# Optimization experiments

Hardware: AMD Instinct MI355X
Metric: run time of the kernel (lower is better)

The kernel has to match this reference:

```python
import jax, jax.numpy as jnp
import numpy as np

EPS = 1e-5

def _mesh_conv_point(f, nbr, w, b):
    # f: [B, C, V] features; nbr: [B, V, K] neighbor vertex indices
    # gather neighbor features per batch: [B, C, V, K]
    g = jax.vmap(lambda fb, nb: fb[:, nb])(f, nbr)
    # prepend self feature -> [B, C, V, K+1]
    x = jnp.concatenate([f[:, :, :, None], g], axis=3)
    # Conv2d with kernel (1, K+1) == contraction over (C, K+1)
    return jnp.einsum('bcvk,ock->bov', x, w) + b[None, :, None]

def _instance_norm(y):
    # InstanceNorm2d (affine=False): normalize over spatial dims (V, 1)
    m = jnp.mean(y, axis=2, keepdims=True)
    v = jnp.var(y, axis=2, keepdims=True)
    return (y - m) * jax.lax.rsqrt(v + EPS)

def setup_inputs() -> dict:
    key = jax.random.key(0)
    k1, k2, k3, k4 = jax.random.split(key, 4)
    B, Cin, Cout, V, K = 4, 64, 128, 50000, 6
    fe = jax.random.normal(k1, (B, Cin, V), dtype=jnp.float32)
    nbrs = jax.random.randint(k2, (B, V, K), 0, V, dtype=jnp.int32)
    w1 = jax.random.normal(k3, (Cout, Cin, K + 1), dtype=jnp.float32) * (1.0 / np.sqrt(Cin * (K + 1)))
    b1 = jnp.zeros((Cout,), dtype=jnp.float32)
    w2 = jax.random.normal(k4, (Cout, Cout, K + 1), dtype=jnp.float32) * (1.0 / np.sqrt(Cout * (K + 1)))
    b2 = jnp.zeros((Cout,), dtype=jnp.float32)
    return {"fe": fe, "nbrs": nbrs, "w1": w1, "b1": b1, "w2": w2, "b2": b2}

def reference(fe, nbrs, w1, b1, w2, b2):
    # conv1 -> instance norm -> relu
    x1 = jax.nn.relu(_instance_norm(_mesh_conv_point(fe, nbrs, w1, b1)))
    # residual block: conv2 -> instance norm -> + x1 -> relu
    x2 = jax.nn.relu(_instance_norm(_mesh_conv_point(x1, nbrs, w2, b2)) + x1)
    # pool=0, so output == before_pool; return the single [B, Cout, V] tensor
    return x2
```

## Files before the change

### kernel.cpp

```cpp
#include <hip/hip_runtime.h>
#include <cstdint>
#include <cstddef>
#include <utility>

typedef unsigned short u16;
typedef u16 u16x8 __attribute__((ext_vector_type(8)));
typedef u16 u16x4 __attribute__((ext_vector_type(4)));
typedef _Float16 f16x8 __attribute__((ext_vector_type(8)));
typedef float f32x4 __attribute__((ext_vector_type(4)));

constexpr int B    = 4;
constexpr int CIN  = 64;
constexpr int COUT = 128;
constexpr int V    = 50000;
constexpr int KP1  = 7;
constexpr float EPS = 1e-5f;

constexpr int BN   = 128;
constexpr int NT   = (V + BN - 1) / BN;
constexpr int NTP  = 392;
constexpr int NT64 = (V + 63) / 64;

__device__ __forceinline__ u16 f2h(float f) {
    _Float16 h = (_Float16)f;
    return __builtin_bit_cast(u16, h);
}
__device__ __forceinline__ float h2f(u16 s) {
    return (float)__builtin_bit_cast(_Float16, s);
}

__device__ __forceinline__ void relusub8(u16x8& a, const u16x8& m) {
    f16x8 af = __builtin_bit_cast(f16x8, a);
    f16x8 mf = __builtin_bit_cast(f16x8, m);
    f16x8 r = af - mf;
#pragma unroll
    for (int j = 0; j < 8; ++j)
        r[j] = (r[j] > (_Float16)0.f) ? r[j] : (_Float16)0.f;
    a = __builtin_bit_cast(u16x8, r);
}

template<int... Is, typename F>
__device__ __forceinline__ void static_for_impl(F&& f, std::integer_sequence<int, Is...>) {
    (f(std::integral_constant<int, Is>{}), ...);
}
template<int N, typename F>
__device__ __forceinline__ void static_for(F&& f) {
    static_for_impl(f, std::make_integer_sequence<int, N>{});
}

template<int C>
__global__ __launch_bounds__(256) void prep_wf(const float* __restrict__ w,
                                               u16* __restrict__ wF) {
    constexpr int RCH = KP1 * C / 32;
    const int g = blockIdx.x * 256 + threadIdx.x;
    if (g >= RCH * 8 * 64) return;
    const int l  = g & 63;
    const int m  = (g >> 6) & 7;
    const int ch = g >> 9;
    const int k  = ch / (C / 32);
    const int c0 = (ch % (C / 32)) * 32;
    const int o  = m * 16 + (l & 15);
    u16x8 out;
#pragma unroll
    for (int j = 0; j < 8; ++j) {
        const int c = c0 + (l >> 4) * 8 + j;
        out[j] = f2h(w[((size_t)o * C + c) * KP1 + k]);
    }
    *(u16x8*)&wF[(size_t)g * 8] = out;
}

__global__ __launch_bounds__(256) void prep_wf_inv(const float* __restrict__ w,
                                                   const float2* __restrict__ S1,
                                                   u16* __restrict__ wF) {
    constexpr int C = COUT;
    constexpr int RCH = KP1 * C / 32;
    const int g  = blockIdx.x * 256 + threadIdx.x;
    const int bb = blockIdx.y;
    if (g >= RCH * 8 * 64) return;
    const int l  = g & 63;
    const int m  = (g >> 6) & 7;
    const int ch = g >> 9;
    const int k  = ch / (C / 32);
    const int c0 = (ch % (C / 32)) * 32;
    const int o  = m * 16 + (l & 15);
    u16x8 out;
#pragma unroll
    for (int j = 0; j < 8; ++j) {
        const int c = c0 + (l >> 4) * 8 + j;
        out[j] = f2h(w[((size_t)o * C + c) * KP1 + k] * S1[bb * COUT + c].y);
    }
    *(u16x8*)&wF[(size_t)bb * RCH * 8 * 64 * 8 + (size_t)g * 8] = out;
}

__global__ __launch_bounds__(256) void transpose_fe(const float* __restrict__ fe,
                                                    u16* __restrict__ feT) {
    __shared__ u16 tile[32][33];
    const int t  = threadIdx.x;
    const int tx = t & 31, ty = t >> 5;
    const int v0 = blockIdx.x * 32;
    const int c0 = blockIdx.y * 32;
    const int b  = blockIdx.z;
#pragma unroll
    for (int p = 0; p < 4; ++p) {
        const int c = c0 + ty + p * 8;
        const int v = v0 + tx;
        if (v < V) tile[ty + p * 8][tx] = f2h(fe[((size_t)b * CIN + c) * V + v]);
    }
    __syncthreads();
#pragma unroll
    for (int p = 0; p < 4; ++p) {
        const int v = v0 + ty + p * 8;
        const int c = c0 + tx;
        if (v < V) feT[((size_t)b * V + v) * CIN + c] = tile[tx][ty + p * 8];
    }
}

template<int C, int OUTL, int NORM>
__global__ __launch_bounds__(256, 2) void conv_mfma(const u16* __restrict__ xin,
                                                    const u16* __restrict__ wF,
                                                    const float* __restrict__ bias,
                                                    const int*  __restrict__ nbr,
                                                    const u16*  __restrict__ mh,
                                                    void* __restrict__ out_,
                                                    float2* __restrict__ P) {
    constexpr int NS = KP1 * C / 64;
    __shared__ __align__(16) u16 Xl[2][BN][72];
    __shared__ __align__(16) u16 Wl[2][8192];
    float2* SredF = (float2*)&Xl[0][0][0];

    const int t    = threadIdx.x;
    const int b    = blockIdx.x / NT;
    const int tile = blockIdx.x % NT;
    const int v0   = tile * BN;
    const int w    = t >> 6;
    const int l    = t & 63;
    const int wo   = (w & 1) * 64;
    const int wv   = (w >> 1) * 64;

    if constexpr (NORM)
        wF += (size_t)b * (KP1 * C / 32) * 8 * 64 * 8;

    const int sv = t >> 1;
    const int h  = t & 1;
    const int vS = v0 + sv;
    int idxS[KP1];
    {
        const int vc = (vS < V) ? vS : 0;
        idxS[0] = vc;
#pragma unroll
        for (int k = 1; k < KP1; ++k)
            idxS[k] = nbr[((size_t)b * V + vc) * 6 + (k - 1)];
    }

    u16x8 mreg[2][4];
    if constexpr (NORM) {
        const u16* mp = mh + b * COUT;
#pragma unroll
        for (int sel = 0; sel < 2; ++sel)
#pragma unroll
            for (int j = 0; j < 4; ++j)
                mreg[sel][j] = *(const u16x8*)&mp[sel * 64 + h * 32 + j * 8];
    }

    int vn[4]; bool ok[4];
#pragma unroll
    for (int n = 0; n < 4; ++n) {
        vn[n] = v0 + wv + n * 16 + (l & 15);
        ok[n] = vn[n] < V;
    }

    f32x4 acc[4][4];
#pragma unroll
    for (int m = 0; m < 4; ++m)
#pragma unroll
        for (int n = 0; n < 4; ++n) acc[m][n] = (f32x4)0.f;

    u16x8 g[4];
    u16x8 wreg[4];

    auto gload = [&](auto SC) {
        constexpr int S    = decltype(SC)::value;
        constexpr int k_   = (C == 64) ? S : (S >> 1);
        constexpr int off_ = (C == 64) ? 0 : (S & 1) * 64;
        const u16* p_ = &xin[((size_t)b * V + idxS[k_]) * C + off_ + h * 32];
#pragma unroll
        for (int j = 0; j < 4; ++j) g[j] = *(const u16x8*)(p_ + j * 8);
    };
    auto wgload = [&](auto SC) {
        constexpr int S = decltype(SC)::value;
        const u16* p_ = wF + (size_t)S * 8192 + t * 32;
#pragma unroll
        for (int j = 0; j < 4; ++j) wreg[j] = *(const u16x8*)(p_ + j * 8);
    };
    auto store = [&](int bufi, auto SC) {
        if constexpr (NORM) {
            constexpr int sel = decltype(SC)::value & 1;
#pragma unroll
            for (int j = 0; j < 4; ++j) relusub8(g[j], mreg[sel][j]);
        }
#pragma unroll
        for (int j = 0; j < 4; ++j)
            *(u16x8*)&Xl[bufi][sv][h * 32 + j * 8] = g[j];
    };
    auto wstore = [&](int bufi) {
#pragma unroll
        for (int j = 0; j < 4; ++j)
            *(u16x8*)&Wl[bufi][t * 32 + j * 8] = wreg[j];
    };

    gload(std::integral_constant<int, 0>{});
    wgload(std::integral_constant<int, 0>{});
    store(0, std::integral_constant<int, 0>{});
    wstore(0);
    asm volatile("s_waitcnt lgkmcnt(0)" ::: "memory");
    __builtin_amdgcn_s_barrier();

    static_for<NS>([&](auto SC) {
        constexpr int s = decltype(SC)::value;
        f16x8 af[8];
#pragma unroll
        for (int kc = 0; kc < 2; ++kc)
#pragma unroll
            for (int m = 0; m < 4; ++m)
                af[kc * 4 + m] =
                    *(const f16x8*)&Wl[s & 1][((kc * 8 + (wo >> 4) + m) * 64 + l) * 8];
        f16x8 bf[4][2];
#pragma unroll
        for (int n = 0; n < 4; ++n)
#pragma unroll
            for (int kc = 0; kc < 2; ++kc)
                bf[n][kc] = *(const f16x8*)&Xl[s & 1][wv + n * 16 + (l & 15)]
                                              [kc * 32 + (l >> 4) * 8];
        if constexpr (s + 1 < NS) {
            wgload(std::integral_constant<int, s + 1>{});
            gload(std::integral_constant<int, s + 1>{});
        }
#pragma unroll
        for (int kc = 0; kc < 2; ++kc)
#pragma unroll
            for (int m = 0; m < 4; ++m)
#pragma unroll
                for (int n = 0; n < 4; ++n)
                    acc[m][n] = __builtin_amdgcn_mfma_f32_16x16x32_f16(af[kc * 4 + m],
                                                                       bf[n][kc],
                                                                       acc[m][n], 0, 0, 0);
        if constexpr (s + 1 < NS) {
            __builtin_amdgcn_sched_barrier(0);
            store((s + 1) & 1, std::integral_constant<int, s + 1>{});
            wstore((s + 1) & 1);
            asm volatile("s_waitcnt lgkmcnt(0)" ::: "memory");
            __builtin_amdgcn_s_barrier();
        }
    });

    if constexpr (OUTL == 0) {
        u16* po = (u16*)out_;
#pragma unroll
        for (int n = 0; n < 4; ++n) {
            if (ok[n]) {
#pragma unroll
                for (int m = 0; m < 4; ++m) {
                    const int o = wo + m * 16 + ((l >> 4) << 2);
                    u16x4 pk;
#pragma unroll
                    for (int q = 0; q < 4; ++q) pk[q] = f2h(acc[m][n][q] + bias[o + q]);
                    *(u16x4*)&po[((size_t)b * V + vn[n]) * COUT + o] = pk;
                }
            }
        }
    } else {
        float* po = (float*)out_;
#pragma unroll
        for (int m = 0; m < 4; ++m) {
            const int o = wo + m * 16 + ((l >> 4) << 2);
#pragma unroll
            for (int q = 0; q < 4; ++q) {
                const float bq = bias[o + q];
#pragma unroll
                for (int n = 0; n < 4; ++n)
                    if (ok[n]) po[((size_t)(b * COUT + o + q)) * V + vn[n]] = acc[m][n][q] + bq;
            }
        }
    }

    __syncthreads();

#pragma unroll
    for (int m = 0; m < 4; ++m) {
        const int o = wo + m * 16 + ((l >> 4) << 2);
        float s[4], s2[4];
#pragma unroll
        for (int q = 0; q < 4; ++q) {
            const float bq = bias[o + q];
            float a = 0.f, aa = 0.f;
#pragma unroll
            for (int n = 0; n < 4; ++n) {
                if (ok[n]) {
                    const float val = acc[m][n][q] + bq;
                    a += val; aa += val * val;
                }
            }
            s[q] = a; s2[q] = aa;
        }
#pragma unroll
        for (int d = 1; d < 16; d <<= 1) {
#pragma unroll
            for (int q = 0; q < 4; ++q) {
                s[q]  += __shfl_xor(s[q],  d, 16);
                s2[q] += __shfl_xor(s2[q], d, 16);
            }
        }
        if ((l & 15) == 0) {
#pragma unroll
            for (int q = 0; q < 4; ++q)
                SredF[w * COUT + o + q] = make_float2(s[q], s2[q]);
        }
    }
    __syncthreads();
    if (t < COUT) {
        const int wlo = t >> 6;
        const float2 a = SredF[wlo * COUT + t];
        const float2 c = SredF[(wlo + 2) * COUT + t];
        P[((size_t)b * COUT + t) * NTP + tile] = make_float2(a.x + c.x, a.y + c.y);
    }
}

__global__ __launch_bounds__(256) void finalize_fused(const float2* __restrict__ P,
                                                      float2* __restrict__ S,
                                                      u16* __restrict__ mh) {
    const int row = blockIdx.x;
    float s = 0.f, s2 = 0.f;
    for (int i = threadIdx.x; i < NT; i += 256) {
        const float2 p = P[(size_t)row * NTP + i];
        s += p.x; s2 += p.y;
    }
    __shared__ float2 red[256];
    red[threadIdx.x] = make_float2(s, s2);
    __syncthreads();
    for (int w = 128; w > 0; w >>= 1) {
        if (threadIdx.x < w) {
            red[threadIdx.x].x += red[threadIdx.x + w].x;
            red[threadIdx.x].y += red[threadIdx.x + w].y;
        }
        __syncthreads();
    }
    if (threadIdx.x == 0) {
        const float m = red[0].x / V;
        const float var = red[0].y / V - m * m;
        S[row] = make_float2(m, rsqrtf(var + EPS));
        if (mh) mh[row] = f2h(m);
    }
}

__global__ __launch_bounds__(256) void final_mix2(const u16* __restrict__ y2,
                                                  const u16* __restrict__ y1,
                                                  const float2* __restrict__ S1,
                                                  const float2* __restrict__ S2,
                                                  float* __restrict__ out) {
    __shared__ float ty[64][33], tx[64][33];
    const int t  = threadIdx.x;
    const int v0 = blockIdx.x * 64;
    const int o0 = blockIdx.y * 32;
    const int b  = blockIdx.z;
    const int jr = (t & 7) * 4;
    const int ir = t >> 3;
#pragma unroll
    for (int p = 0; p < 2; ++p) {
        const int i = ir + p * 32;
        const int v = v0 + i;
        if (v < V) {
            const size_t base = ((size_t)b * V + v) * COUT + o0 + jr;
            const u16x4 a = *(const u16x4*)&y2[base];
            const u16x4 c = *(const u16x4*)&y1[base];
#pragma unroll
            for (int q = 0; q < 4; ++q) {
                const float2 s1 = S1[b * COUT + o0 + jr + q];
                ty[i][jr + q] = h2f(a[q]);
                tx[i][jr + q] = s1.y * fmaxf(h2f(c[q]) - s1.x, 0.f);
            }
        }
    }
    __syncthreads();
    const int vl = t & 63, v = v0 + vl, oo0 = t >> 6;
    if (v < V) {
#pragma unroll
        for (int p = 0; p < 8; ++p) {
            const int oo = oo0 + p * 4;
            const int o  = o0 + oo;
            const float2 s = S2[b * COUT + o];
            out[((size_t)b * COUT + o) * V + v] =
                fmaxf((ty[vl][oo] - s.x) * s.y + tx[vl][oo], 0.f);
        }
    }
}

__global__ __launch_bounds__(256) void final_mix(float* __restrict__ y,
                                                 const u16* __restrict__ y1,
                                                 const float2* __restrict__ S1,
                                                 const float2* __restrict__ S2) {
    __shared__ float tile[64][33];
    const int t  = threadIdx.x;
    const int v0 = blockIdx.x * 64;
    const int o0 = blockIdx.y * 32;
    const int b  = blockIdx.z;
    const int j  = t & 31;
    const int i0 = t >> 5;
    const float2 s1 = S1[b * COUT + o0 + j];
#pragma unroll
    for (int p = 0; p < 8; ++p) {
        const int i = i0 + p * 8;
        const int v = v0 + i;
        tile[i][j] = (v < V)
            ? s1.y * fmaxf(h2f(y1[((size_t)b * V + v) * COUT + o0 + j]) - s1.x, 0.f)
            : 0.f;
    }
    __syncthreads();
    const int vl  = t & 63;
    const int v   = v0 + vl;
    const int oo0 = t >> 6;
    if (v < V) {
#pragma unroll
        for (int p = 0; p < 8; ++p) {
            const int oo = oo0 + p * 4;
            const int o  = o0 + oo;
            const size_t idx = ((size_t)b * COUT + o) * V + v;
            const float2 s = S2[b * COUT + o];
            const float f = (y[idx] - s.x) * s.y + tile[vl][oo];
            y[idx] = fmaxf(f, 0.f);
        }
    }
}

extern "C" void kernel_launch(void* const* d_in, const int* in_sizes, int n_in,
                              void* d_out, int out_size, void* d_ws, size_t ws_size,
                              hipStream_t stream) {
    const float* fe  = (const float*)d_in[0];
    const int*   nbr = (const int*)d_in[1];
    const float* w1  = (const float*)d_in[2];
    const float* b1  = (const float*)d_in[3];
    const float* w2  = (const float*)d_in[4];
    const float* b2  = (const float*)d_in[5];
    float* outf = (float*)d_out;
    char*  ws   = (char*)d_ws;

    constexpr size_t wF1_b = (size_t)(KP1 * CIN  / 32) * 8 * 64 * 8 * 2;
    constexpr size_t wF2_b = (size_t)B * (KP1 * COUT / 32) * 8 * 64 * 8 * 2;
    constexpr size_t S_b   = (size_t)B * COUT * 8;
    constexpr size_t mh_b  = ((size_t)B * COUT * 2 + 255) & ~255ull;
    constexpr size_t Pf_b  = (size_t)B * COUT * NTP * 8;
    constexpr size_t x1_b  = (size_t)B * V * COUT * 2;
    constexpr size_t y2_b  = (size_t)B * V * COUT * 2;
    constexpr size_t feT_b = (size_t)B * V * CIN * 2;
    const size_t base = wF1_b + wF2_b + 2 * S_b + mh_b + Pf_b;

    const bool full = (ws_size >= base + x1_b + y2_b);
    const bool t3   = (ws_size >= base + x1_b + feT_b);
    const bool t4   = (ws_size >= base + x1_b);
    if (!full && !t3 && !t4) return;

    size_t off = 0;
    u16*    wF1 = (u16*)(ws + off);    off += wF1_b;
    u16*    wF2 = (u16*)(ws + off);    off += wF2_b;
    float2* S1  = (float2*)(ws + off); off += S_b;
    float2* S2  = (float2*)(ws + off); off += S_b;
    u16*    mh1 = (u16*)(ws + off);    off += mh_b;
    float2* P   = (float2*)(ws + off); off += Pf_b;
    u16*    x1  = (u16*)(ws + off);    off += x1_b;
    u16*    ext = (u16*)(ws + off);

    u16* feT = (full || t3) ? ext : (u16*)d_out;

    prep_wf<CIN><<<(KP1 * CIN / 32) * 8 * 64 / 256, 256, 0, stream>>>(w1, wF1);

    dim3 gt((V + 31) / 32, CIN / 32, B);
    transpose_fe<<<gt, 256, 0, stream>>>(fe, feT);

    conv_mfma<CIN, 0, 0><<<B * NT, 256, 0, stream>>>(feT, wF1, b1, nbr, nullptr, x1, P);
    finalize_fused<<<B * COUT, 256, 0, stream>>>(P, S1, mh1);

    dim3 gw((KP1 * COUT / 32) * 8 * 64 / 256, B);
    prep_wf_inv<<<gw, 256, 0, stream>>>(w2, S1, wF2);

    dim3 gf(NT64, COUT / 32, B);
    if (full) {
        u16* y2 = ext;
        conv_mfma<COUT, 0, 1><<<B * NT, 256, 0, stream>>>(x1, wF2, b2, nbr, mh1, y2, P);
        finalize_fused<<<B * COUT, 256, 0, stream>>>(P, S2, nullptr);
        final_mix2<<<gf, 256, 0, stream>>>(y2, x1, S1, S2, outf);
    } else {
        conv_mfma<COUT, 1, 1><<<B * NT, 256, 0, stream>>>(x1, wF2, b2, nbr, mh1, outf, P);
        finalize_fused<<<B * COUT, 256, 0, stream>>>(P, S2, nullptr);
        final_mix<<<gf, 256, 0, stream>>>(outf, x1, S1, S2);
    }
}
```

Baseline: 254.2 us.

## Load MFMA weight fragments directly from global and deepen gather prefetch

```diff
diff --git a/kernel.cpp b/kernel.cpp
--- a/kernel.cpp
+++ b/kernel.cpp
@@ -125,8 +125,7 @@
                                                     float2* __restrict__ P) {
     constexpr int NS = KP1 * C / 64;
     __shared__ __align__(16) u16 Xl[2][BN][72];
-    __shared__ __align__(16) u16 Wl[2][8192];
-    float2* SredF = (float2*)&Xl[0][0][0];
+    __shared__ float2 Sred[4][COUT];
 
     const int t    = threadIdx.x;
     const int b    = blockIdx.x / NT;
@@ -175,55 +174,46 @@
 #pragma unroll
         for (int n = 0; n < 4; ++n) acc[m][n] = (f32x4)0.f;
 
-    u16x8 g[4];
-    u16x8 wreg[4];
-
-    auto gload = [&](auto SC) {
+    u16x8 g[2][4];
+    f16x8 af[2][8];
+
+    auto gload = [&](auto SC, u16x8 (&gr)[4]) {
         constexpr int S    = decltype(SC)::value;
         constexpr int k_   = (C == 64) ? S : (S >> 1);
         constexpr int off_ = (C == 64) ? 0 : (S & 1) * 64;
         const u16* p_ = &xin[((size_t)b * V + idxS[k_]) * C + off_ + h * 32];
 #pragma unroll
-        for (int j = 0; j < 4; ++j) g[j] = *(const u16x8*)(p_ + j * 8);
+        for (int j = 0; j < 4; ++j) gr[j] = *(const u16x8*)(p_ + j * 8);
     };
-    auto wgload = [&](auto SC) {
+    auto aload = [&](auto SC, f16x8 (&ar)[8]) {
         constexpr int S = decltype(SC)::value;
-        const u16* p_ = wF + (size_t)S * 8192 + t * 32;
-#pragma unroll
-        for (int j = 0; j < 4; ++j) wreg[j] = *(const u16x8*)(p_ + j * 8);
+#pragma unroll
+        for (int kc = 0; kc < 2; ++kc)
+#pragma unroll
+            for (int m = 0; m < 4; ++m)
+                ar[kc * 4 + m] =
+                    *(const f16x8*)&wF[(((size_t)(2 * S + kc) * 8 + (wo >> 4) + m) * 64 + l) * 8];
     };
-    auto store = [&](int bufi, auto SC) {
+    auto store = [&](int bufi, u16x8 (&gr)[4], auto SC) {
         if constexpr (NORM) {
             constexpr int sel = decltype(SC)::value & 1;
 #pragma unroll
-            for (int j = 0; j < 4; ++j) relusub8(g[j], mreg[sel][j]);
+            for (int j = 0; j < 4; ++j) relusub8(gr[j], mreg[sel][j]);
         }
 #pragma unroll
         for (int j = 0; j < 4; ++j)
-            *(u16x8*)&Xl[bufi][sv][h * 32 + j * 8] = g[j];
+            *(u16x8*)&Xl[bufi][sv][h * 32 + j * 8] = gr[j];
     };
-    auto wstore = [&](int bufi) {
-#pragma unroll
-        for (int j = 0; j < 4; ++j)
-            *(u16x8*)&Wl[bufi][t * 32 + j * 8] = wreg[j];
-    };
-
-    gload(std::integral_constant<int, 0>{});
-    wgload(std::integral_constant<int, 0>{});
-    store(0, std::integral_constant<int, 0>{});
-    wstore(0);
+
+    gload(std::integral_constant<int, 0>{}, g[0]);
+    if constexpr (NS > 1) gload(std::integral_constant<int, 1>{}, g[1]);
+    aload(std::integral_constant<int, 0>{}, af[0]);
+    store(0, g[0], std::integral_constant<int, 0>{});
     asm volatile("s_waitcnt lgkmcnt(0)" ::: "memory");
     __builtin_amdgcn_s_barrier();
 
     static_for<NS>([&](auto SC) {
         constexpr int s = decltype(SC)::value;
-        f16x8 af[8];
-#pragma unroll
-        for (int kc = 0; kc < 2; ++kc)
-#pragma unroll
-            for (int m = 0; m < 4; ++m)
-                af[kc * 4 + m] =
-                    *(const f16x8*)&Wl[s & 1][((kc * 8 + (wo >> 4) + m) * 64 + l) * 8];
         f16x8 bf[4][2];
 #pragma unroll
         for (int n = 0; n < 4; ++n)
@@ -231,23 +221,22 @@
             for (int kc = 0; kc < 2; ++kc)
                 bf[n][kc] = *(const f16x8*)&Xl[s & 1][wv + n * 16 + (l & 15)]
                                               [kc * 32 + (l >> 4) * 8];
-        if constexpr (s + 1 < NS) {
-            wgload(std::integral_constant<int, s + 1>{});
-            gload(std::integral_constant<int, s + 1>{});
-        }
+        if constexpr (s + 2 < NS)
+            gload(std::integral_constant<int, s + 2>{}, g[s & 1]);
+        if constexpr (s + 1 < NS)
+            aload(std::integral_constant<int, s + 1>{}, af[(s + 1) & 1]);
 #pragma unroll
         for (int kc = 0; kc < 2; ++kc)
 #pragma unroll
             for (int m = 0; m < 4; ++m)
 #pragma unroll
                 for (int n = 0; n < 4; ++n)
-                    acc[m][n] = __builtin_amdgcn_mfma_f32_16x16x32_f16(af[kc * 4 + m],
+                    acc[m][n] = __builtin_amdgcn_mfma_f32_16x16x32_f16(af[s & 1][kc * 4 + m],
                                                                        bf[n][kc],
                                                                        acc[m][n], 0, 0, 0);
         if constexpr (s + 1 < NS) {
             __builtin_amdgcn_sched_barrier(0);
-            store((s + 1) & 1, std::integral_constant<int, s + 1>{});
-            wstore((s + 1) & 1);
+            store((s + 1) & 1, g[(s + 1) & 1], std::integral_constant<int, s + 1>{});
             asm volatile("s_waitcnt lgkmcnt(0)" ::: "memory");
             __builtin_amdgcn_s_barrier();
         }
@@ -282,8 +271,6 @@
             }
         }
     }
-
-    __syncthreads();
 
 #pragma unroll
     for (int m = 0; m < 4; ++m) {
@@ -313,14 +300,14 @@
         if ((l & 15) == 0) {
 #pragma unroll
             for (int q = 0; q < 4; ++q)
-                SredF[w * COUT + o + q] = make_float2(s[q], s2[q]);
+                Sred[w][o + q] = make_float2(s[q], s2[q]);
         }
     }
     __syncthreads();
     if (t < COUT) {
         const int wlo = t >> 6;
-        const float2 a = SredF[wlo * COUT + t];
-        const float2 c = SredF[(wlo + 2) * COUT + t];
+        const float2 a = Sred[wlo][t];
+        const float2 c = Sred[wlo + 2][t];
         P[((size_t)b * COUT + t) * NTP + tile] = make_float2(a.x + c.x, a.y + c.y);
     }
 }
```

Result: faster. 224.3 us (-11.8%).
